# Kernel optimization log

Hardware: AMD Instinct MI355X
Metric: run time of the kernel (lower is better)

## Reference

```python
import jax, jax.numpy as jnp
import numpy as np

ORDER = 3  # cubic B-splines, matching BSpline(..., 3)


def bspline_basis(x, t, order):
    """Cox-de Boor recursion, vectorized over batch and features.

    x: [B, F] evaluation points
    t: [F, M] sorted knot vectors (M = num_basis + order + 1)
    returns: [B, F, M-1-order] basis values B_j^{order}(x), zero outside the
    base interval [t[order], t[M-1-order]] (scipy extrapolate=False + nan_to_num).
    """
    M = t.shape[-1]
    xd = x[:, :, None]            # [B, F, 1]
    tb = t[None, :, :]            # [1, F, M]
    # degree-0 indicator functions: [B, F, M-1]
    B = ((xd >= tb[:, :, :-1]) & (xd < tb[:, :, 1:])).astype(x.dtype)
    for d in range(1, order + 1):
        t0 = tb[:, :, : M - d - 1]   # t_j
        td = tb[:, :, d : M - 1]     # t_{j+d}
        t1 = tb[:, :, 1 : M - d]     # t_{j+1}
        td1 = tb[:, :, d + 1 : M]    # t_{j+d+1}
        den1 = td - t0
        den2 = td1 - t1
        w1 = jnp.where(den1 > 0, (xd - t0) / jnp.where(den1 > 0, den1, 1.0), 0.0)
        w2 = jnp.where(den2 > 0, (td1 - xd) / jnp.where(den2 > 0, den2, 1.0), 0.0)
        B = w1 * B[:, :, : M - d - 1] + w2 * B[:, :, 1 : M - d]
    # zero outside the base interval [t[order], t[n]] (scipy NaN -> nan_to_num -> 0)
    lo = t[None, :, order]           # [1, F]
    hi = t[None, :, M - 1 - order]   # [1, F]
    valid = ((x >= lo) & (x <= hi)).astype(x.dtype)  # [B, F]
    return B * valid[:, :, None]


def setup_inputs() -> dict:
    key = jax.random.key(0)
    k_x, k_w, k_b = jax.random.split(key, 3)
    batch, in_features, out_features, num_basis = 4096, 512, 512, 30
    x = jax.random.normal(k_x, (batch, in_features), dtype=jnp.float32)
    knots = jnp.broadcast_to(
        jnp.linspace(-2.0, 2.0, num_basis + ORDER + 1, dtype=jnp.float32),
        (in_features, num_basis + ORDER + 1),
    )
    weights = jax.random.normal(k_w, (out_features, in_features, num_basis), dtype=jnp.float32)
    bias = jax.random.normal(k_b, (out_features,), dtype=jnp.float32)
    return {"x": x, "knots": knots, "weights": weights, "bias": bias}


def reference(x, knots, weights, bias):
    ks = jnp.sort(knots, axis=-1)              # module sorts knots before eval
    basis = bspline_basis(x, ks, ORDER)        # [B, F, num_basis]
    out = jnp.einsum("bij,kij->bk", basis, weights)
    return out + bias
```

## Files before the change

### kernel.cpp

```cpp
#include <hip/hip_runtime.h>
#include <hip/hip_bf16.h>
#include <stdint.h>


#define BATCH 4096
#define INF   512
#define OUTF  512
#define NB    30
#define NBP   32
#define NKNOT 34
#define KDIMP (INF * NBP)

#define BM 128
#define BN 128
#define BK 64
#define KSPLIT 8
#define KCHUNK (KDIMP / KSPLIT)
#define NT     (KCHUNK / BK)
#define FPC    (KCHUNK / NBP)

typedef short v8s __attribute__((ext_vector_type(8)));
typedef float v4f __attribute__((ext_vector_type(4)));

__device__ __forceinline__ unsigned short f2bf(float f) {
  uint32_t u = __float_as_uint(f);
  uint32_t r = (u + 0x7fffu + ((u >> 16) & 1u)) >> 16;
  return (unsigned short)r;
}

__device__ __forceinline__ void gload16(const unsigned short* g, unsigned short* l) {
  auto gp = reinterpret_cast<const __attribute__((address_space(1))) unsigned short*>(
      reinterpret_cast<uintptr_t>(g));
  auto lp = reinterpret_cast<__attribute__((address_space(3))) unsigned short*>(
      reinterpret_cast<uintptr_t>(l));
  __builtin_amdgcn_global_load_lds(gp, lp, 16, 0, 0);
}

__device__ __forceinline__ v8s place4(uint64_t v, int d) {
  int s = d * 16;
  uint32_t ud = (uint32_t)d;
  uint64_t vls    = v << (s & 63);
  uint64_t vrs_hi = v >> ((64 - s) & 63);
  uint64_t vrs_lo = v >> ((-s) & 63);
  uint64_t lo = (ud <= 3u) ? vls : (((uint32_t)(-d) - 1u) <= 2u ? vrs_lo : 0ull);
  uint64_t hi = ((ud - 1u) <= 2u) ? vrs_hi : (((ud - 4u) <= 3u) ? vls : 0ull);
  union { uint32_t u[4]; v8s s8; } r;
  r.u[0] = (uint32_t)lo; r.u[1] = (uint32_t)(lo >> 32);
  r.u[2] = (uint32_t)hi; r.u[3] = (uint32_t)(hi >> 32);
  return r.s8;
}

__global__ __launch_bounds__(256) void w_cast_kernel(const float* __restrict__ in,
                                                     unsigned short* __restrict__ out) {
  int idx = blockIdx.x * 256 + threadIdx.x;
  int k   = idx >> 13;
  int rem = idx & 8191;
  int i   = rem >> 4;
  int jp  = rem & 15;
  int j   = jp * 2;
  const float* src = in + ((size_t)k * INF + i) * NB;
  float lo = (j     < NB) ? src[j]     : 0.f;
  float hi = (j + 1 < NB) ? src[j + 1] : 0.f;
  ((uint32_t*)out)[idx] = (uint32_t)f2bf(lo) | ((uint32_t)f2bf(hi) << 16);
}

__global__ __launch_bounds__(256) void basis_kernel(const float* __restrict__ x,
                                                    const float* __restrict__ knots,
                                                    uint4* __restrict__ valsJ) {
  __shared__ float tile[32][33];
  int b0 = blockIdx.x * 32;
  int f0 = blockIdx.y * 32;
  int lx = threadIdx.x & 31;
  int ly = threadIdx.x >> 5;
  #pragma unroll
  for (int q = 0; q < 4; ++q)
    tile[ly + q * 8][lx] = x[(size_t)(b0 + ly + q * 8) * INF + f0 + lx];
  __syncthreads();
  #pragma unroll
  for (int q = 0; q < 4; ++q) {
    int fy = ly + q * 8;
    float xv = tile[lx][fy];
    const float* tk = knots + (size_t)(f0 + fy) * NKNOT;
    uint4 pv = {0u, 0u, 0u, 0u};
    float tlo = tk[3], thi = tk[30];
    if (xv >= tlo && xv <= thi) {
      float t0v = tk[0];
      float h   = tk[1] - t0v;
      int m = (int)floorf((xv - t0v) * __builtin_amdgcn_rcpf(h));
      m = m < 3 ? 3 : (m > 30 ? 30 : m);
      while (m > 3 && xv < tk[m]) --m;
      while (m < 30 && xv >= tk[m + 1]) ++m;
      float Nv[4], left[4], right[4];
      Nv[0] = 1.f;
      #pragma unroll
      for (int d = 1; d <= 3; ++d) {
        left[d]  = xv - tk[m + 1 - d];
        right[d] = tk[m + d] - xv;
        float saved = 0.f;
        #pragma unroll
        for (int r = 0; r < d; ++r) {
          float temp = Nv[r] * __builtin_amdgcn_rcpf(right[r + 1] + left[d - r]);
          Nv[r] = saved + right[r + 1] * temp;
          saved = left[d - r] * temp;
        }
        Nv[d] = saved;
      }
      pv.x = (uint32_t)f2bf(Nv[0]) | ((uint32_t)f2bf(Nv[1]) << 16);
      pv.y = (uint32_t)f2bf(Nv[2]) | ((uint32_t)f2bf(Nv[3]) << 16);
      pv.z = (uint32_t)(m - 3);
    }
    valsJ[(size_t)(f0 + fy) * BATCH + b0 + lx] = pv;
  }
}

__global__ __launch_bounds__(256) void bias_kernel(const float* __restrict__ bias,
                                                   float* __restrict__ out) {
  int idx = blockIdx.x * 256 + threadIdx.x;
  out[idx] = bias[idx & (OUTF - 1)];
}

__global__ __launch_bounds__(256, 3) void gemm_kernel(const uint4* __restrict__ valsJ,
                                                      const unsigned short* __restrict__ Bt,
                                                      float* __restrict__ C) {
  __shared__ unsigned short Bs[2][BN * BK];
  int tid  = threadIdx.x;
  int lane = tid & 63;
  int w    = tid >> 6;

  int bid = blockIdx.x;
  int swz = (bid & 7) * 128 + (bid >> 3);
  int bn  = swz >> 8;
  int rem = swz & 255;
  int ks  = rem >> 5;
  int bm  = rem & 31;

  int row0 = bm * BM;
  int col0 = bn * BN;
  int kk0  = ks * KCHUNK;
  int fbase = ks * FPC;

  int wr  = (w >> 1) & 1;
  int wc  = w & 1;
  int r16 = lane & 15;
  int kg  = lane >> 4;

  int lrow = lane >> 3;
  int lseg = (lane & 7) ^ lrow;
  const unsigned short* gb = Bt + (size_t)(col0 + w * 8 + lrow) * KDIMP + kk0 + lseg * 8;

  unsigned s0   = ((unsigned)kg ^ (unsigned)(r16 & 7)) << 4;
  unsigned boff = (unsigned)(wc * 64 + r16) * 128;

  const uint4* vbase = valsJ + (size_t)fbase * BATCH + row0 + wr * 64 + r16;

  v4f acc[4][4];
  #pragma unroll
  for (int i = 0; i < 4; ++i)
    #pragma unroll
    for (int j = 0; j < 4; ++j)
      acc[i][j] = (v4f){0.f, 0.f, 0.f, 0.f};

  uint4 pf[8];
  #pragma unroll
  for (int mi = 0; mi < 4; ++mi)
    #pragma unroll
    for (int hfi = 0; hfi < 2; ++hfi)
      pf[mi * 2 + hfi] = vbase[(size_t)hfi * BATCH + mi * 16];
  #pragma unroll
  for (int q = 0; q < 4; ++q)
    gload16(gb + (size_t)q * (32 * KDIMP), &Bs[0][w * 512 + q * 2048]);
  __syncthreads();

  for (int t = 0; t < NT; ++t) {
    int c = t & 1;
    v8s af[2][4];
    #pragma unroll
    for (int mi = 0; mi < 4; ++mi)
      #pragma unroll
      for (int kc = 0; kc < 2; ++kc) {
        uint4 p = pf[mi * 2 + kc];
        uint64_t v = (uint64_t)p.x | ((uint64_t)p.y << 32);
        af[kc][mi] = place4(v, (int)p.z - kg * 8);
      }
    if (t + 1 < NT) {
      const unsigned short* src = gb + (size_t)(t + 1) * BK;
      #pragma unroll
      for (int q = 0; q < 4; ++q)
        gload16(src + (size_t)q * (32 * KDIMP), &Bs[c ^ 1][w * 512 + q * 2048]);
      size_t fo = (size_t)(2 * (t + 1)) * BATCH;
      #pragma unroll
      for (int mi = 0; mi < 4; ++mi)
        #pragma unroll
        for (int hfi = 0; hfi < 2; ++hfi)
          pf[mi * 2 + hfi] = vbase[fo + (size_t)hfi * BATCH + mi * 16];
    }
    const char* Bb = (const char*)Bs[c];
    #pragma unroll
    for (int kc = 0; kc < 2; ++kc) {
      unsigned sk = s0 ^ (unsigned)(kc << 6);
      v8s bf[4];
      #pragma unroll
      for (int ni = 0; ni < 4; ++ni)
        bf[ni] = *(const v8s*)(Bb + boff + ni * 2048 + sk);
      #pragma unroll
      for (int mi = 0; mi < 4; ++mi)
        #pragma unroll
        for (int ni = 0; ni < 4; ++ni)
          acc[mi][ni] = __builtin_amdgcn_mfma_f32_16x16x32_bf16(af[kc][mi], bf[ni], acc[mi][ni], 0, 0, 0);
    }
    __syncthreads();
  }

  int crow = (lane >> 4) * 4;
  int ccol = lane & 15;
  #pragma unroll
  for (int mi = 0; mi < 4; ++mi) {
    #pragma unroll
    for (int ni = 0; ni < 4; ++ni) {
      int r = row0 + wr * 64 + mi * 16 + crow;
      int c = col0 + wc * 64 + ni * 16 + ccol;
      #pragma unroll
      for (int q = 0; q < 4; ++q)
        atomicAdd(&C[(size_t)(r + q) * OUTF + c], acc[mi][ni][q]);
    }
  }
}

extern "C" void kernel_launch(void* const* d_in, const int* in_sizes, int n_in,
                              void* d_out, int out_size, void* d_ws, size_t ws_size,
                              hipStream_t stream) {
  const float* x     = (const float*)d_in[0];
  const float* knots = (const float*)d_in[1];
  const float* W     = (const float*)d_in[2];
  const float* bias  = (const float*)d_in[3];
  float* out = (float*)d_out;

  unsigned short* Wt    = (unsigned short*)d_ws;
  uint4*          valsJ = (uint4*)((char*)d_ws + (size_t)OUTF * KDIMP * 2);

  w_cast_kernel<<<(OUTF * KDIMP / 2) / 256, 256, 0, stream>>>(W, Wt);
  basis_kernel<<<dim3(BATCH / 32, INF / 32), 256, 0, stream>>>(x, knots, valsJ);
  bias_kernel<<<(BATCH * OUTF) / 256, 256, 0, stream>>>(bias, out);
  gemm_kernel<<<(BATCH / BM) * (OUTF / BN) * KSPLIT, 256, 0, stream>>>(valsJ, Wt, out);
}
```

Measured before the change: 215.8 us.

## Enlarge GEMM tile to 256x256 with LDS-staged sparse A and phased MFMA schedule

The GEMM block tile grows from 128x128 to 256x256 with 512 threads (8 waves, each computing a 128x64 subtile). Sparse basis values are no longer expanded in registers per wave; each thread writes its row of zero-filled A into a swizzled, double-buffered LDS tile that all waves share. The k-step is split into four phases separated by barriers with s_setprio around the MFMA groups, so global B loads and the prefetch of the next A entry interleave with compute. This aims to raise reuse per loaded byte and cut redundant A expansion, at the cost of more LDS, more registers, fewer blocks (256 total) and extra barriers.

Measured after the change: 206.4 us. -4.4%, faster.

```diff
diff --git a/kernel.cpp b/kernel.cpp
--- a/kernel.cpp
+++ b/kernel.cpp
@@ -11,12 +11,12 @@
 #define NKNOT 34
 #define KDIMP (INF * NBP)
 
-#define BM 128
-#define BN 128
+#define BM 256
+#define BN 256
 #define BK 64
 #define KSPLIT 8
 #define KCHUNK (KDIMP / KSPLIT)
-#define NT     (KCHUNK / BK)
+#define NSTEPS (KCHUNK / BK)
 #define FPC    (KCHUNK / NBP)
 
 typedef short v8s __attribute__((ext_vector_type(8)));
@@ -34,20 +34,6 @@
   auto lp = reinterpret_cast<__attribute__((address_space(3))) unsigned short*>(
       reinterpret_cast<uintptr_t>(l));
   __builtin_amdgcn_global_load_lds(gp, lp, 16, 0, 0);
-}
-
-__device__ __forceinline__ v8s place4(uint64_t v, int d) {
-  int s = d * 16;
-  uint32_t ud = (uint32_t)d;
-  uint64_t vls    = v << (s & 63);
-  uint64_t vrs_hi = v >> ((64 - s) & 63);
-  uint64_t vrs_lo = v >> ((-s) & 63);
-  uint64_t lo = (ud <= 3u) ? vls : (((uint32_t)(-d) - 1u) <= 2u ? vrs_lo : 0ull);
-  uint64_t hi = ((ud - 1u) <= 2u) ? vrs_hi : (((ud - 4u) <= 3u) ? vls : 0ull);
-  union { uint32_t u[4]; v8s s8; } r;
-  r.u[0] = (uint32_t)lo; r.u[1] = (uint32_t)(lo >> 32);
-  r.u[2] = (uint32_t)hi; r.u[3] = (uint32_t)(hi >> 32);
-  return r.s8;
 }
 
 __global__ __launch_bounds__(256) void w_cast_kernel(const float* __restrict__ in,
@@ -119,105 +105,152 @@
   out[idx] = bias[idx & (OUTF - 1)];
 }
 
-__global__ __launch_bounds__(256, 3) void gemm_kernel(const uint4* __restrict__ valsJ,
+__device__ __forceinline__ void writeA(unsigned short* Abuf, int eb, int hf, uint4 p) {
+  unsigned rowb = (unsigned)eb * 128;
+  unsigned x7   = (unsigned)(eb & 7);
+  char* base = (char*)Abuf;
+  uint4 z = {0u, 0u, 0u, 0u};
+  #pragma unroll
+  for (int s = 0; s < 4; ++s) {
+    unsigned slot = ((unsigned)(hf * 4 + s)) ^ x7;
+    *(uint4*)(base + rowb + (slot << 4)) = z;
+  }
+  int j0 = (int)p.z;
+  int d0 = hf * 16 + (j0 >> 1);
+  #define WR32(d, val) { unsigned by = (unsigned)(d) * 4u; \
+    *(uint32_t*)(base + rowb + ((((by >> 4) ^ x7) << 4) | (by & 15u))) = (val); }
+  if (j0 & 1) {
+    WR32(d0,     p.x << 16);
+    WR32(d0 + 1, (p.x >> 16) | (p.y << 16));
+    WR32(d0 + 2, p.y >> 16);
+  } else {
+    WR32(d0,     p.x);
+    WR32(d0 + 1, p.y);
+  }
+  #undef WR32
+}
+
+__global__ __launch_bounds__(512, 2) void gemm_kernel(const uint4* __restrict__ valsJ,
                                                       const unsigned short* __restrict__ Bt,
                                                       float* __restrict__ C) {
+  __shared__ unsigned short As[2][BM * BK];
   __shared__ unsigned short Bs[2][BN * BK];
   int tid  = threadIdx.x;
   int lane = tid & 63;
   int w    = tid >> 6;
 
   int bid = blockIdx.x;
-  int swz = (bid & 7) * 128 + (bid >> 3);
-  int bn  = swz >> 8;
-  int rem = swz & 255;
-  int ks  = rem >> 5;
-  int bm  = rem & 31;
+  int swz = (bid & 7) * 32 + (bid >> 3);
+  int bn  = swz >> 7;
+  int ks  = (swz >> 4) & 7;
+  int bm  = swz & 15;
 
   int row0 = bm * BM;
   int col0 = bn * BN;
   int kk0  = ks * KCHUNK;
   int fbase = ks * FPC;
 
-  int wr  = (w >> 1) & 1;
-  int wc  = w & 1;
+  int wr  = w >> 2;
+  int wc  = w & 3;
   int r16 = lane & 15;
   int kg  = lane >> 4;
 
+  int eb = tid & 255;
+  int hf = tid >> 8;
+  const uint4* vb = valsJ + ((size_t)(fbase + hf) * BATCH + row0 + eb);
+
   int lrow = lane >> 3;
   int lseg = (lane & 7) ^ lrow;
-  const unsigned short* gb = Bt + (size_t)(col0 + w * 8 + lrow) * KDIMP + kk0 + lseg * 8;
+  const unsigned short* gb = Bt + (size_t)(col0 + w * 8 + lrow) * KDIMP + lseg * 8;
 
   unsigned s0   = ((unsigned)kg ^ (unsigned)(r16 & 7)) << 4;
+  unsigned aoff = (unsigned)(wr * 128 + r16) * 128;
   unsigned boff = (unsigned)(wc * 64 + r16) * 128;
 
-  const uint4* vbase = valsJ + (size_t)fbase * BATCH + row0 + wr * 64 + r16;
-
-  v4f acc[4][4];
-  #pragma unroll
-  for (int i = 0; i < 4; ++i)
+  v4f acc[8][4];
+  #pragma unroll
+  for (int i = 0; i < 8; ++i)
     #pragma unroll
     for (int j = 0; j < 4; ++j)
       acc[i][j] = (v4f){0.f, 0.f, 0.f, 0.f};
 
-  uint4 pf[8];
-  #pragma unroll
-  for (int mi = 0; mi < 4; ++mi)
-    #pragma unroll
-    for (int hfi = 0; hfi < 2; ++hfi)
-      pf[mi * 2 + hfi] = vbase[(size_t)hfi * BATCH + mi * 16];
-  #pragma unroll
-  for (int q = 0; q < 4; ++q)
-    gload16(gb + (size_t)q * (32 * KDIMP), &Bs[0][w * 512 + q * 2048]);
+  {
+    uint4 vc = vb[0];
+    writeA(&As[0][0], eb, hf, vc);
+    const unsigned short* g0 = gb + kk0;
+    #pragma unroll
+    for (int pr = 0; pr < 4; ++pr)
+      gload16(g0 + (size_t)pr * 64 * KDIMP, &Bs[0][pr * 4096 + w * 512]);
+  }
+  uint4 vn = vb[(size_t)2 * BATCH];
   __syncthreads();
 
-  for (int t = 0; t < NT; ++t) {
-    int c = t & 1;
-    v8s af[2][4];
-    #pragma unroll
-    for (int mi = 0; mi < 4; ++mi)
-      #pragma unroll
-      for (int kc = 0; kc < 2; ++kc) {
-        uint4 p = pf[mi * 2 + kc];
-        uint64_t v = (uint64_t)p.x | ((uint64_t)p.y << 32);
-        af[kc][mi] = place4(v, (int)p.z - kg * 8);
-      }
-    if (t + 1 < NT) {
-      const unsigned short* src = gb + (size_t)(t + 1) * BK;
-      #pragma unroll
-      for (int q = 0; q < 4; ++q)
-        gload16(src + (size_t)q * (32 * KDIMP), &Bs[c ^ 1][w * 512 + q * 2048]);
-      size_t fo = (size_t)(2 * (t + 1)) * BATCH;
-      #pragma unroll
-      for (int mi = 0; mi < 4; ++mi)
-        #pragma unroll
-        for (int hfi = 0; hfi < 2; ++hfi)
-          pf[mi * 2 + hfi] = vbase[fo + (size_t)hfi * BATCH + mi * 16];
+  for (int t = 0; t < NSTEPS; ++t) {
+    int p = t & 1;
+    bool stage = (t + 1 < NSTEPS);
+    unsigned short* An = &As[p ^ 1][0];
+    unsigned short* Bn = &Bs[p ^ 1][0];
+    const unsigned short* gsrc = gb + (size_t)(kk0 + (t + 1) * BK);
+    if (stage) writeA(An, eb, hf, vn);
+
+    const char* Ab = (const char*)&As[p][0];
+    const char* Bb = (const char*)&Bs[p][0];
+    v8s bf[2][4];
+    uint4 vn2;
+    #pragma unroll
+    for (int mq = 0; mq < 4; ++mq) {
+      if (mq == 0) {
+        #pragma unroll
+        for (int kc = 0; kc < 2; ++kc)
+          #pragma unroll
+          for (int ni = 0; ni < 4; ++ni)
+            bf[kc][ni] = *(const v8s*)(Bb + boff + ni * 2048 + (s0 ^ (kc << 6)));
+      }
+      v8s af[2][2];
+      #pragma unroll
+      for (int q = 0; q < 2; ++q)
+        #pragma unroll
+        for (int kc = 0; kc < 2; ++kc)
+          af[q][kc] = *(const v8s*)(Ab + aoff + (mq * 2 + q) * 2048 + (s0 ^ (kc << 6)));
+      if (stage) {
+        if (mq == 0) {
+          gload16(gsrc,                        Bn + w * 512);
+          gload16(gsrc + (size_t) 64 * KDIMP,  Bn +  4096 + w * 512);
+        } else if (mq == 1) {
+          gload16(gsrc + (size_t)128 * KDIMP,  Bn +  8192 + w * 512);
+        } else if (mq == 2) {
+          gload16(gsrc + (size_t)192 * KDIMP,  Bn + 12288 + w * 512);
+        }
+      }
+      if (mq == 1) {
+        int s2 = (t + 2 < NSTEPS) ? (t + 2) : (NSTEPS - 1);
+        vn2 = vb[(size_t)2 * s2 * BATCH];
+      }
+      __builtin_amdgcn_s_barrier();
+      __builtin_amdgcn_s_setprio(1);
+      #pragma unroll
+      for (int q = 0; q < 2; ++q)
+        #pragma unroll
+        for (int kc = 0; kc < 2; ++kc)
+          #pragma unroll
+          for (int ni = 0; ni < 4; ++ni)
+            acc[mq * 2 + q][ni] = __builtin_amdgcn_mfma_f32_16x16x32_bf16(
+                af[q][kc], bf[kc][ni], acc[mq * 2 + q][ni], 0, 0, 0);
+      __builtin_amdgcn_s_setprio(0);
+      if (mq < 3) __builtin_amdgcn_s_barrier();
     }
-    const char* Bb = (const char*)Bs[c];
-    #pragma unroll
-    for (int kc = 0; kc < 2; ++kc) {
-      unsigned sk = s0 ^ (unsigned)(kc << 6);
-      v8s bf[4];
-      #pragma unroll
-      for (int ni = 0; ni < 4; ++ni)
-        bf[ni] = *(const v8s*)(Bb + boff + ni * 2048 + sk);
-      #pragma unroll
-      for (int mi = 0; mi < 4; ++mi)
-        #pragma unroll
-        for (int ni = 0; ni < 4; ++ni)
-          acc[mi][ni] = __builtin_amdgcn_mfma_f32_16x16x32_bf16(af[kc][mi], bf[ni], acc[mi][ni], 0, 0, 0);
-    }
-    __syncthreads();
+    asm volatile("s_waitcnt vmcnt(0) lgkmcnt(0)" ::: "memory");
+    __builtin_amdgcn_s_barrier();
+    vn = vn2;
   }
 
   int crow = (lane >> 4) * 4;
   int ccol = lane & 15;
   #pragma unroll
-  for (int mi = 0; mi < 4; ++mi) {
+  for (int mi = 0; mi < 8; ++mi) {
     #pragma unroll
     for (int ni = 0; ni < 4; ++ni) {
-      int r = row0 + wr * 64 + mi * 16 + crow;
+      int r = row0 + wr * 128 + mi * 16 + crow;
       int c = col0 + wc * 64 + ni * 16 + ccol;
       #pragma unroll
       for (int q = 0; q < 4; ++q)
@@ -241,5 +274,5 @@
   w_cast_kernel<<<(OUTF * KDIMP / 2) / 256, 256, 0, stream>>>(W, Wt);
   basis_kernel<<<dim3(BATCH / 32, INF / 32), 256, 0, stream>>>(x, knots, valsJ);
   bias_kernel<<<(BATCH * OUTF) / 256, 256, 0, stream>>>(bias, out);
-  gemm_kernel<<<(BATCH / BM) * (OUTF / BN) * KSPLIT, 256, 0, stream>>>(valsJ, Wt, out);
-}
+  gemm_kernel<<<(BATCH / BM) * (OUTF / BN) * KSPLIT, 512, 0, stream>>>(valsJ, Wt, out);
+}
```

## Build A tile in LDS from sparse basis records and halve K-split

Applied to the files above, without the earlier changes.

Instead of each wave expanding its compressed basis records into MFMA A-fragments in registers with the shift-heavy place4, each thread now writes one record's four nonzeros into a swizzled, zero-filled A tile in LDS, and waves read A-fragments from LDS. This removes the duplicated expansion work. KSPLIT drops from 8 to 4, halving the atomicAdd traffic to the output and doubling the K loop length per block. It also adds s_setprio around the MFMA section and a two-barrier scheme with a single A buffer. The trade is extra LDS writes and barriers per iteration, plus half as many blocks.

After: 189.0 us. 1.14x faster.

```diff
diff --git a/kernel.cpp b/kernel.cpp
--- a/kernel.cpp
+++ b/kernel.cpp
@@ -14,7 +14,7 @@
 #define BM 128
 #define BN 128
 #define BK 64
-#define KSPLIT 8
+#define KSPLIT 4
 #define KCHUNK (KDIMP / KSPLIT)
 #define NT     (KCHUNK / BK)
 #define FPC    (KCHUNK / NBP)
@@ -34,20 +34,6 @@
   auto lp = reinterpret_cast<__attribute__((address_space(3))) unsigned short*>(
       reinterpret_cast<uintptr_t>(l));
   __builtin_amdgcn_global_load_lds(gp, lp, 16, 0, 0);
-}
-
-__device__ __forceinline__ v8s place4(uint64_t v, int d) {
-  int s = d * 16;
-  uint32_t ud = (uint32_t)d;
-  uint64_t vls    = v << (s & 63);
-  uint64_t vrs_hi = v >> ((64 - s) & 63);
-  uint64_t vrs_lo = v >> ((-s) & 63);
-  uint64_t lo = (ud <= 3u) ? vls : (((uint32_t)(-d) - 1u) <= 2u ? vrs_lo : 0ull);
-  uint64_t hi = ((ud - 1u) <= 2u) ? vrs_hi : (((ud - 4u) <= 3u) ? vls : 0ull);
-  union { uint32_t u[4]; v8s s8; } r;
-  r.u[0] = (uint32_t)lo; r.u[1] = (uint32_t)(lo >> 32);
-  r.u[2] = (uint32_t)hi; r.u[3] = (uint32_t)(hi >> 32);
-  return r.s8;
 }
 
 __global__ __launch_bounds__(256) void w_cast_kernel(const float* __restrict__ in,
@@ -119,18 +105,44 @@
   out[idx] = bias[idx & (OUTF - 1)];
 }
 
+__device__ __forceinline__ void writeA(unsigned short* Abuf, int eb, int hf, uint4 p) {
+  unsigned rowb = (unsigned)eb * 128;
+  unsigned x7   = (unsigned)(eb & 7);
+  char* base = (char*)Abuf;
+  uint4 z = {0u, 0u, 0u, 0u};
+  #pragma unroll
+  for (int s = 0; s < 4; ++s) {
+    unsigned slot = ((unsigned)(hf * 4 + s)) ^ x7;
+    *(uint4*)(base + rowb + (slot << 4)) = z;
+  }
+  int j0 = (int)p.z;
+  int d0 = hf * 16 + (j0 >> 1);
+  #define WR32(d, val) { unsigned by = (unsigned)(d) * 4u; \
+    *(uint32_t*)(base + rowb + ((((by >> 4) ^ x7) << 4) | (by & 15u))) = (val); }
+  if (j0 & 1) {
+    WR32(d0,     p.x << 16);
+    WR32(d0 + 1, (p.x >> 16) | (p.y << 16));
+    WR32(d0 + 2, p.y >> 16);
+  } else {
+    WR32(d0,     p.x);
+    WR32(d0 + 1, p.y);
+  }
+  #undef WR32
+}
+
 __global__ __launch_bounds__(256, 3) void gemm_kernel(const uint4* __restrict__ valsJ,
                                                       const unsigned short* __restrict__ Bt,
                                                       float* __restrict__ C) {
+  __shared__ unsigned short As[BM * BK];
   __shared__ unsigned short Bs[2][BN * BK];
   int tid  = threadIdx.x;
   int lane = tid & 63;
   int w    = tid >> 6;
 
   int bid = blockIdx.x;
-  int swz = (bid & 7) * 128 + (bid >> 3);
-  int bn  = swz >> 8;
-  int rem = swz & 255;
+  int swz = (bid & 7) * 64 + (bid >> 3);
+  int bn  = swz >> 7;
+  int rem = swz & 127;
   int ks  = rem >> 5;
   int bm  = rem & 31;
 
@@ -144,14 +156,17 @@
   int r16 = lane & 15;
   int kg  = lane >> 4;
 
+  int eb = tid & 127;
+  int hf = tid >> 7;
+  const uint4* vb = valsJ + ((size_t)(fbase + hf) * BATCH + row0 + eb);
+
   int lrow = lane >> 3;
   int lseg = (lane & 7) ^ lrow;
   const unsigned short* gb = Bt + (size_t)(col0 + w * 8 + lrow) * KDIMP + kk0 + lseg * 8;
 
   unsigned s0   = ((unsigned)kg ^ (unsigned)(r16 & 7)) << 4;
+  unsigned aoff = (unsigned)(wr * 64 + r16) * 128;
   unsigned boff = (unsigned)(wc * 64 + r16) * 128;
-
-  const uint4* vbase = valsJ + (size_t)fbase * BATCH + row0 + wr * 64 + r16;
 
   v4f acc[4][4];
   #pragma unroll
@@ -160,45 +175,38 @@
     for (int j = 0; j < 4; ++j)
       acc[i][j] = (v4f){0.f, 0.f, 0.f, 0.f};
 
-  uint4 pf[8];
-  #pragma unroll
-  for (int mi = 0; mi < 4; ++mi)
-    #pragma unroll
-    for (int hfi = 0; hfi < 2; ++hfi)
-      pf[mi * 2 + hfi] = vbase[(size_t)hfi * BATCH + mi * 16];
-  #pragma unroll
-  for (int q = 0; q < 4; ++q)
-    gload16(gb + (size_t)q * (32 * KDIMP), &Bs[0][w * 512 + q * 2048]);
-  __syncthreads();
+  {
+    uint4 vc = vb[0];
+    writeA(As, eb, hf, vc);
+    #pragma unroll
+    for (int q = 0; q < 4; ++q)
+      gload16(gb + (size_t)q * (32 * KDIMP), &Bs[0][w * 512 + q * 2048]);
+  }
+  uint4 vn = vb[2 * BATCH];
+  asm volatile("s_waitcnt vmcnt(0) lgkmcnt(0)" ::: "memory");
+  __builtin_amdgcn_s_barrier();
 
   for (int t = 0; t < NT; ++t) {
     int c = t & 1;
-    v8s af[2][4];
-    #pragma unroll
-    for (int mi = 0; mi < 4; ++mi)
-      #pragma unroll
-      for (int kc = 0; kc < 2; ++kc) {
-        uint4 p = pf[mi * 2 + kc];
-        uint64_t v = (uint64_t)p.x | ((uint64_t)p.y << 32);
-        af[kc][mi] = place4(v, (int)p.z - kg * 8);
-      }
     if (t + 1 < NT) {
       const unsigned short* src = gb + (size_t)(t + 1) * BK;
       #pragma unroll
       for (int q = 0; q < 4; ++q)
         gload16(src + (size_t)q * (32 * KDIMP), &Bs[c ^ 1][w * 512 + q * 2048]);
-      size_t fo = (size_t)(2 * (t + 1)) * BATCH;
-      #pragma unroll
-      for (int mi = 0; mi < 4; ++mi)
-        #pragma unroll
-        for (int hfi = 0; hfi < 2; ++hfi)
-          pf[mi * 2 + hfi] = vbase[fo + (size_t)hfi * BATCH + mi * 16];
-    }
+    }
+    uint4 vn2 = vn;
+    if (t + 2 < NT) vn2 = vb[(size_t)(2 * (t + 2)) * BATCH];
+
+    const char* Ab = (const char*)As;
     const char* Bb = (const char*)Bs[c];
+    __builtin_amdgcn_s_setprio(1);
     #pragma unroll
     for (int kc = 0; kc < 2; ++kc) {
       unsigned sk = s0 ^ (unsigned)(kc << 6);
-      v8s bf[4];
+      v8s af[4], bf[4];
+      #pragma unroll
+      for (int mi = 0; mi < 4; ++mi)
+        af[mi] = *(const v8s*)(Ab + aoff + mi * 2048 + sk);
       #pragma unroll
       for (int ni = 0; ni < 4; ++ni)
         bf[ni] = *(const v8s*)(Bb + boff + ni * 2048 + sk);
@@ -206,9 +214,14 @@
       for (int mi = 0; mi < 4; ++mi)
         #pragma unroll
         for (int ni = 0; ni < 4; ++ni)
-          acc[mi][ni] = __builtin_amdgcn_mfma_f32_16x16x32_bf16(af[kc][mi], bf[ni], acc[mi][ni], 0, 0, 0);
-    }
-    __syncthreads();
+          acc[mi][ni] = __builtin_amdgcn_mfma_f32_16x16x32_bf16(af[mi], bf[ni], acc[mi][ni], 0, 0, 0);
+    }
+    __builtin_amdgcn_s_setprio(0);
+    __builtin_amdgcn_s_barrier();
+    if (t + 1 < NT) writeA(As, eb, hf, vn);
+    asm volatile("s_waitcnt vmcnt(0) lgkmcnt(0)" ::: "memory");
+    __builtin_amdgcn_s_barrier();
+    vn = vn2;
   }
 
   int crow = (lane >> 4) * 4;
```
